# Kernel tuning notes

Hardware: AMD Instinct MI355X
Metric: run time of the kernel (lower is better)

The kernel has to match this reference:

```python
import jax, jax.numpy as jnp
import numpy as np

HID = 64        # HID_DIM of seq2seq encoder
NL = 2          # N_LAYERS
D = HID * NL    # dim_hidden = 128
TYPES = 16      # node op types; Input=0, Const=1
MAX_ET = 32     # max edge_type id
NUM_ROUNDS = 2


def _gru_cell(x, h, Wih, Whh, bih, bhh):
    # torch GRU gate ordering: r, z, n
    gi = x @ Wih.T + bih
    gh = h @ Whh.T + bhh
    ir, iz, inn = jnp.split(gi, 3, axis=-1)
    hr, hz, hn = jnp.split(gh, 3, axis=-1)
    r = jax.nn.sigmoid(ir + hr)
    z = jax.nn.sigmoid(iz + hz)
    n = jnp.tanh(inn + r * hn)
    return (1.0 - z) * n + z * h


def _posenc(n, d):
    pos = jnp.arange(n, dtype=jnp.float32)[:, None]
    i = jnp.arange(d // 2, dtype=jnp.float32)[None, :]
    inv = jnp.exp(-jnp.log(10000.0) * (2.0 * i / d))
    pe = jnp.zeros((n, d), jnp.float32)
    pe = pe.at[:, 0::2].set(jnp.sin(pos * inv))
    pe = pe.at[:, 1::2].set(jnp.cos(pos * inv))
    return pe


def _forward(x, edge_index, edge_type, sim_res, seq_len,
             enc_Wih0, enc_Whh0, enc_bih0, enc_bhh0,
             enc_Wih1, enc_Whh1, enc_bih1, enc_bhh1,
             Wq, Wk, Wv, op_emb, mlp_W1, mlp_b1, mlp_W2, mlp_b2,
             gru_Wih, gru_Whh, gru_bih, gru_bhh):
    N = x.shape[0]
    # --- seq2seq encode (2-layer GRU over time), computed for all nodes then masked ---
    xs = jnp.swapaxes(sim_res[:, :seq_len, :], 0, 1)  # [T, N, W]
    h0 = jnp.zeros((N, HID), sim_res.dtype)
    h1 = jnp.zeros((N, HID), sim_res.dtype)

    def step(carry, xt):
        h0, h1 = carry
        h0 = _gru_cell(xt, h0, enc_Wih0, enc_Whh0, enc_bih0, enc_bhh0)
        h1 = _gru_cell(h0, h1, enc_Wih1, enc_Whh1, enc_bih1, enc_bhh1)
        return (h0, h1), None

    (h0, h1), _ = jax.lax.scan(step, (h0, h1), xs)
    enc = jnp.concatenate([h0, h1], axis=-1)  # [N, D] = permute(1,0,2).flatten(1)
    mask = (x[:, 0] == 1) | (x[:, 1] == 1)    # Input | Const nodes
    node_emb = jnp.where(mask[:, None], enc, 0.0)

    src, dst = edge_index[0], edge_index[1]
    edge_op = jnp.argmax(x[dst], axis=1)       # [E]
    pe = _posenc(MAX_ET, D)
    edge_feat = pe[edge_type] + op_emb[edge_op]  # [E, D]
    scale = 1.0 / jnp.sqrt(jnp.float32(D))

    for _ in range(NUM_ROUNDS):
        kf = node_emb[src] + edge_feat         # [E, D]
        q = node_emb[dst] @ Wq.T
        k = kf @ Wk.T
        v = kf @ Wv.T
        score = jnp.sum(q * k, axis=-1) * scale  # [E]
        m = jax.ops.segment_max(score, dst, num_segments=N)
        ex = jnp.exp(score - m[dst])
        den = jax.ops.segment_sum(ex, dst, num_segments=N)
        alpha = ex / (den[dst] + 1e-9)
        aggr = jax.ops.segment_sum(alpha[:, None] * v, dst, num_segments=N)  # [N, D]
        aggr = jax.nn.relu(aggr @ mlp_W1.T + mlp_b1) @ mlp_W2.T + mlp_b2
        node_emb = _gru_cell(aggr, node_emb, gru_Wih, gru_Whh, gru_bih, gru_bhh)
    return node_emb


def setup_inputs() -> dict:
    key = jax.random.key(0)
    ks = jax.random.split(key, 24)
    N, E, T, W = 20000, 320000, 32, 32
    s = 0.05

    def g(k, shape):
        return jax.random.normal(k, shape, dtype=jnp.float32) * s

    node_type = jax.random.randint(ks[0], (N,), 0, TYPES)
    x = jax.nn.one_hot(node_type, TYPES, dtype=jnp.float32)
    edge_index = jax.random.randint(ks[1], (2, E), 0, N)
    edge_type = jax.random.randint(ks[2], (E,), 0, MAX_ET)
    sim_res = jax.random.uniform(ks[3], (N, T, W), dtype=jnp.float32)
    return {
        "x": x, "edge_index": edge_index, "edge_type": edge_type,
        "sim_res": sim_res, "seq_len": 32,
        "enc_Wih0": g(ks[4], (3 * HID, W)), "enc_Whh0": g(ks[5], (3 * HID, HID)),
        "enc_bih0": g(ks[6], (3 * HID,)), "enc_bhh0": g(ks[7], (3 * HID,)),
        "enc_Wih1": g(ks[8], (3 * HID, HID)), "enc_Whh1": g(ks[9], (3 * HID, HID)),
        "enc_bih1": g(ks[10], (3 * HID,)), "enc_bhh1": g(ks[11], (3 * HID,)),
        "Wq": g(ks[12], (D, D)), "Wk": g(ks[13], (D, D)), "Wv": g(ks[14], (D, D)),
        "op_emb": g(ks[15], (TYPES, D)),
        "mlp_W1": g(ks[16], (D, D)), "mlp_b1": g(ks[17], (D,)),
        "mlp_W2": g(ks[18], (D, D)), "mlp_b2": g(ks[19], (D,)),
        "gru_Wih": g(ks[20], (3 * D, D)), "gru_Whh": g(ks[21], (3 * D, D)),
        "gru_bih": g(ks[22], (3 * D,)), "gru_bhh": g(ks[23], (3 * D,)),
    }


def reference(x, edge_index, edge_type, sim_res, seq_len,
              enc_Wih0, enc_Whh0, enc_bih0, enc_bhh0,
              enc_Wih1, enc_Whh1, enc_bih1, enc_bhh1,
              Wq, Wk, Wv, op_emb, mlp_W1, mlp_b1, mlp_W2, mlp_b2,
              gru_Wih, gru_Whh, gru_bih, gru_bhh):
    return _forward(x, edge_index, edge_type, sim_res, seq_len,
                    enc_Wih0, enc_Whh0, enc_bih0, enc_bhh0,
                    enc_Wih1, enc_Whh1, enc_bih1, enc_bhh1,
                    Wq, Wk, Wv, op_emb, mlp_W1, mlp_b1, mlp_W2, mlp_b2,
                    gru_Wih, gru_Whh, gru_bih, gru_bhh)
```

## Files before the change

### kernel.cpp

```cpp
#include <hip/hip_runtime.h>

typedef unsigned int uint;
typedef unsigned short ushort;

typedef __attribute__((ext_vector_type(8))) short bf8;
typedef __attribute__((ext_vector_type(4))) float f32x4;
typedef _Float16 half_t;
typedef __attribute__((ext_vector_type(8))) half_t h8;

__device__ __forceinline__ ushort f2bf(float f){
  uint u = __builtin_bit_cast(uint, f);
  u = u + 0x7FFFu + ((u >> 16) & 1u);
  return (ushort)(u >> 16);
}
__device__ __forceinline__ float bfl(uint u){ return __builtin_bit_cast(float, u << 16); }
__device__ __forceinline__ float bfh(uint u){ return __builtin_bit_cast(float, u & 0xFFFF0000u); }
__device__ __forceinline__ uint pkhalf(float a, float b){
  ushort lo = __builtin_bit_cast(ushort, (half_t)a);
  ushort hi = __builtin_bit_cast(ushort, (half_t)b);
  return (uint)lo | ((uint)hi << 16);
}
__device__ __forceinline__ float sigmoidf_(float x){ return 1.0f/(1.0f + __expf(-x)); }
__device__ __forceinline__ float tanhf_(float x){
  x = fminf(15.0f, fmaxf(-15.0f, x));
  float t = __expf(-2.0f*x);
  return (1.0f - t)/(1.0f + t);
}
__device__ __forceinline__ f32x4 mfma_f16(h8 a, h8 b, f32x4 c){
  return __builtin_amdgcn_mfma_f32_16x16x32_f16(a, b, c, 0, 0, 0);
}
__device__ __forceinline__ f32x4 mfma_bf(bf8 a, bf8 b, f32x4 c){
  return __builtin_amdgcn_mfma_f32_16x16x32_bf16(a, b, c, 0, 0, 0);
}
__device__ __forceinline__ h8 ldw8(const float* p){
  f32x4 a = *(const f32x4*)p, b = *(const f32x4*)(p+4);
  h8 v;
  #pragma unroll
  for (int j=0;j<4;j++){ v[j] = (half_t)a[j]; v[4+j] = (half_t)b[j]; }
  return v;
}

__global__ __launch_bounds__(256) void k_prep(const float* __restrict__ x,
    const int* __restrict__ dst,
    int* __restrict__ typ, int* __restrict__ mlist, int* __restrict__ cnt,
    int* __restrict__ deg, float* __restrict__ Hf, ushort* __restrict__ Hb,
    int N, int E){
  int i = blockIdx.x*256 + threadIdx.x;
  int total = gridDim.x*256;
  if (i < N){
    const float* xr = x + (size_t)i*16;
    int t = 0;
    #pragma unroll
    for (int j=0;j<16;j++) if (xr[j] > 0.5f) t = j;
    typ[i] = t;
    if (t < 2){
      int p = atomicAdd(cnt, 1);
      mlist[p] = i;
    }
  }
  if (i < E) atomicAdd(&deg[dst[i]], 1);
  f32x4 z4 = (f32x4)0.0f;
  for (int j = i; j < N*32; j += total) ((f32x4*)Hf)[j] = z4;
  uint2 z2; z2.x = 0u; z2.y = 0u;
  for (int j = i; j < N*32; j += total) ((uint2*)Hb)[j] = z2;
}

__global__ __launch_bounds__(256) void k_cvt(
    const float* wq, const float* wk, const float* wv,
    const float* w1, const float* w2, const float* wih, const float* whh,
    const float* __restrict__ op_emb,
    ushort* oqkv, ushort* o1, ushort* o2, ushort* oih, ushort* ohh,
    ushort* __restrict__ EF){
  int i = blockIdx.x*256 + threadIdx.x;
  int stride = gridDim.x*256;
  for (int j=i; j<16384; j+=stride){
    oqkv[j]       = f2bf(wq[j]);
    oqkv[16384+j] = f2bf(wk[j]);
    oqkv[32768+j] = f2bf(wv[j]);
    o1[j] = f2bf(w1[j]);
    o2[j] = f2bf(w2[j]);
  }
  for (int j=i; j<49152; j+=stride){ oih[j]=f2bf(wih[j]); ohh[j]=f2bf(whh[j]); }
  for (int idx=i; idx<512*128; idx+=stride){
    int r = idx >> 7, d = idx & 127;
    int et = r >> 4, op = r & 15;
    int j = d >> 1;
    float inv = __expf(-0.1439115683f * (float)j);
    float ang = (float)et * inv;
    float v = (d & 1) ? __cosf(ang) : __sinf(ang);
    EF[idx] = f2bf(v + op_emb[op*128 + d]);
  }
}

template<int RELU, int HASBIAS>
__global__ __launch_bounds__(256) void k_gemm(
    const ushort* __restrict__ A, const ushort* __restrict__ B,
    const float* __restrict__ bias, ushort* __restrict__ C, int M, int N){
  int lane = threadIdx.x & 63, wv = threadIdx.x >> 6;
  int tM = blockIdx.x*64 + (wv>>1)*32;
  int tN = blockIdx.y*64 + (wv&1)*32;
  int r16 = lane & 15, kg = (lane>>4)*8;
  f32x4 acc[2][2];
  #pragma unroll
  for (int i=0;i<2;i++)
    #pragma unroll
    for (int j=0;j<2;j++) acc[i][j] = (f32x4)0.0f;
  #pragma unroll
  for (int k0=0;k0<128;k0+=32){
    bf8 a[2], b[2];
    #pragma unroll
    for (int i=0;i<2;i++){
      int row = tM + i*16 + r16; if (row > M-1) row = M-1;
      a[i] = *(const bf8*)(A + (size_t)row*128 + k0 + kg);
    }
    #pragma unroll
    for (int j=0;j<2;j++){
      int col = tN + j*16 + r16;
      b[j] = *(const bf8*)(B + (size_t)col*128 + k0 + kg);
    }
    #pragma unroll
    for (int i=0;i<2;i++)
      #pragma unroll
      for (int j=0;j<2;j++)
        acc[i][j] = __builtin_amdgcn_mfma_f32_16x16x32_bf16(a[i], b[j], acc[i][j], 0, 0, 0);
  }
  #pragma unroll
  for (int i=0;i<2;i++)
    #pragma unroll
    for (int j=0;j<2;j++){
      int col = tN + j*16 + r16;
      float bs = HASBIAS ? bias[col] : 0.0f;
      #pragma unroll
      for (int q=0;q<4;q++){
        int row = tM + i*16 + (lane>>4)*4 + q;
        if (row < M){
          float v = acc[i][j][q] + bs;
          if (RELU) v = fmaxf(v, 0.0f);
          C[(size_t)row*N + col] = f2bf(v);
        }
      }
    }
}

__global__ __launch_bounds__(512, 1) void k_enc4(
    const float* __restrict__ sim_res, const int* __restrict__ seqlen,
    const float* __restrict__ Wih0, const float* __restrict__ Whh0,
    const float* __restrict__ bih0, const float* __restrict__ bhh0,
    const float* __restrict__ Wih1, const float* __restrict__ Whh1,
    const float* __restrict__ bih1, const float* __restrict__ bhh1,
    const int* __restrict__ mlist, const int* __restrict__ cntp,
    float* __restrict__ Hf, ushort* __restrict__ Hb){
  int C = *cntp;
  int base = blockIdx.x * 16;
  if (C == 0 || base >= C) return;
  int tid = threadIdx.x;
  int w = tid >> 6, l = tid & 63;
  int node = l & 15, hi = l >> 4;
  int grp = w >> 2;
  int ws  = w & 3;

  __shared__ int nod[16];
  __shared__ __align__(16) float  Xs[16*32*32];
  __shared__ __align__(16) ushort H0h[2][16*64], H1h[2][16*64];

  if (tid < 16){
    int idx = base + tid;
    nod[tid] = mlist[idx < C ? idx : C-1];
  }
  for (int i = tid; i < 16*64; i += 512){
    H0h[0][i] = 0; H0h[1][i] = 0; H1h[0][i] = 0; H1h[1][i] = 0;
  }
  __syncthreads();

  for (int m = tid; m < 4096; m += 512){
    int nm = m >> 8, tt = (m >> 3) & 31, c = m & 7;
    int cs = c ^ (nm & 7);
    f32x4 v = *(const f32x4*)(sim_res + (size_t)nod[nm]*1024 + tt*32 + cs*4);
    *(f32x4*)(Xs + m*4) = v;
  }

  int rr = 16*ws + node;
  h8 zf;
  #pragma unroll
  for (int j=0;j<8;j++) zf[j] = (half_t)0.f;
  h8 Ai_r[2] = {zf, zf}, Ai_z[2] = {zf, zf}, Ai_n[2] = {zf, zf};
  h8 Ah_r[2], Ah_z[2], Ah_n[2];
  if (grp == 0){
    Ai_r[0] = ldw8(Wih0 + (size_t)rr*32        + hi*8);
    Ai_z[0] = ldw8(Wih0 + (size_t)(64+rr)*32   + hi*8);
    Ai_n[0] = ldw8(Wih0 + (size_t)(128+rr)*32  + hi*8);
    #pragma unroll
    for (int s=0;s<2;s++){
      Ah_r[s] = ldw8(Whh0 + (size_t)rr*64       + s*32 + hi*8);
      Ah_z[s] = ldw8(Whh0 + (size_t)(64+rr)*64  + s*32 + hi*8);
      Ah_n[s] = ldw8(Whh0 + (size_t)(128+rr)*64 + s*32 + hi*8);
    }
  } else {
    #pragma unroll
    for (int s=0;s<2;s++){
      Ai_r[s] = ldw8(Wih1 + (size_t)rr*64       + s*32 + hi*8);
      Ai_z[s] = ldw8(Wih1 + (size_t)(64+rr)*64  + s*32 + hi*8);
      Ai_n[s] = ldw8(Wih1 + (size_t)(128+rr)*64 + s*32 + hi*8);
      Ah_r[s] = ldw8(Whh1 + (size_t)rr*64       + s*32 + hi*8);
      Ah_z[s] = ldw8(Whh1 + (size_t)(64+rr)*64  + s*32 + hi*8);
      Ah_n[s] = ldw8(Whh1 + (size_t)(128+rr)*64 + s*32 + hi*8);
    }
  }
  const float* bi = grp ? bih1 : bih0;
  const float* bh = grp ? bhh1 : bhh0;
  float br[4], bz[4], bni[4], bnh[4];
  #pragma unroll
  for (int q=0;q<4;q++){
    int row = 16*ws + hi*4 + q;
    br[q]  = bi[row]      + bh[row];
    bz[q]  = bi[64+row]   + bh[64+row];
    bni[q] = bi[128+row];
    bnh[q] = bh[128+row];
  }

  int T = *seqlen; if (T > 32) T = 32; if (T < 0) T = 0;
  float hm[4] = {0.f, 0.f, 0.f, 0.f};

  const int swz = (node & 7) << 4;
  const int wo  = node * 128;
  const int wba = 32*ws + 8*hi;
  const int rd0 = wo + ((16*hi) ^ swz);
  const int rd1 = wo + ((64 + 16*hi) ^ swz);
  const int xc0 = (2*hi)   ^ (node & 7);
  const int xc1 = (2*hi+1) ^ (node & 7);
  const float* xrow = Xs + node*1024;

  __syncthreads();

  for (int k = 0; k <= T; ++k){
    int cur = k & 1;
    bool act = grp ? (k >= 1) : (k < T);
    if (act){
      h8 in0 = zf, in1 = zf, st0, st1;
      if (grp == 0){
        f32x4 xa = *(const f32x4*)(xrow + k*32 + xc0*4);
        f32x4 xb = *(const f32x4*)(xrow + k*32 + xc1*4);
        #pragma unroll
        for (int j=0;j<4;j++){ in0[j] = (half_t)xa[j]; in0[4+j] = (half_t)xb[j]; }
        st0 = *(const h8*)((const char*)H0h[cur] + rd0);
        st1 = *(const h8*)((const char*)H0h[cur] + rd1);
      } else {
        in0 = *(const h8*)((const char*)H0h[cur] + rd0);
        in1 = *(const h8*)((const char*)H0h[cur] + rd1);
        st0 = *(const h8*)((const char*)H1h[cur] + rd0);
        st1 = *(const h8*)((const char*)H1h[cur] + rd1);
      }
      f32x4 ar = {br[0],br[1],br[2],br[3]};
      f32x4 az = {bz[0],bz[1],bz[2],bz[3]};
      f32x4 an = {bni[0],bni[1],bni[2],bni[3]};
      f32x4 hn = {bnh[0],bnh[1],bnh[2],bnh[3]};
      ar = mfma_f16(Ai_r[0], in0, ar);
      az = mfma_f16(Ai_z[0], in0, az);
      an = mfma_f16(Ai_n[0], in0, an);
      if (grp){
        ar = mfma_f16(Ai_r[1], in1, ar);
        az = mfma_f16(Ai_z[1], in1, az);
        an = mfma_f16(Ai_n[1], in1, an);
      }
      ar = mfma_f16(Ah_r[0], st0, ar); ar = mfma_f16(Ah_r[1], st1, ar);
      az = mfma_f16(Ah_z[0], st0, az); az = mfma_f16(Ah_z[1], st1, az);
      hn = mfma_f16(Ah_n[0], st0, hn); hn = mfma_f16(Ah_n[1], st1, hn);
      #pragma unroll
      for (int q=0;q<4;q++){
        float r = sigmoidf_(ar[q]);
        float z = sigmoidf_(az[q]);
        float n = tanhf_(an[q] + r*hn[q]);
        hm[q] = (1.f - z)*n + z*hm[q];
      }
      char* outb = grp ? (char*)H1h[cur^1] : (char*)H0h[cur^1];
      *(uint*)(outb + wo + ( wba      ^ swz)) = pkhalf(hm[0], hm[1]);
      *(uint*)(outb + wo + ((wba + 4) ^ swz)) = pkhalf(hm[2], hm[3]);
    }
    __syncthreads();
  }

  if (base + node < C){
    int nd = nod[node];
    int off = grp ? 64 : 0;
    #pragma unroll
    for (int q=0;q<4;q++){
      int j = off + 16*ws + hi*4 + q;
      Hf[(size_t)nd*128 + j] = hm[q];
      Hb[(size_t)nd*128 + j] = f2bf(hm[q]);
    }
  }
}

__global__ __launch_bounds__(1024) void k_scan(const int* __restrict__ deg,
    int* __restrict__ rowptr, int* __restrict__ cursor, int N){
  __shared__ int wsum[16];
  __shared__ int carry_s;
  int tid = threadIdx.x, lane = tid & 63, wid = tid >> 6;
  if (tid == 0) carry_s = 0;
  __syncthreads();
  int nch = (N + 1023) / 1024;
  for (int c=0; c<nch; ++c){
    int i = c*1024 + tid;
    int v = (i < N) ? deg[i] : 0;
    int x = v;
    #pragma unroll
    for (int off=1; off<64; off<<=1){
      int t = __shfl_up(x, off, 64);
      if (lane >= off) x += t;
    }
    if (lane == 63) wsum[wid] = x;
    __syncthreads();
    int base = carry_s;
    int woff = 0;
    for (int w2=0; w2<wid; ++w2) woff += wsum[w2];
    int excl = base + woff + x - v;
    if (i < N){ rowptr[i] = excl; cursor[i] = excl; }
    __syncthreads();
    if (tid == 0){
      int s = 0;
      for (int w2=0; w2<16; ++w2) s += wsum[w2];
      carry_s = base + s;
    }
    __syncthreads();
  }
  if (tid == 0) rowptr[N] = carry_s;
}

__global__ __launch_bounds__(256) void k_scatter(const int* __restrict__ src,
    const int* __restrict__ dst, const int* __restrict__ etype, const int* __restrict__ typ,
    int* __restrict__ cursor, int* __restrict__ es_src, int* __restrict__ es_tab, int E){
  int e = blockIdx.x*256 + threadIdx.x;
  if (e < E){
    int d = dst[e];
    int pos = atomicAdd(&cursor[d], 1);
    es_src[pos] = src[e];
    es_tab[pos] = etype[e]*16 + typ[d];
  }
}

__global__ __launch_bounds__(256) void k_attn(
    const uint* __restrict__ QKV, const uint* __restrict__ KVT,
    const int* __restrict__ rowptr, const int* __restrict__ es_src, const int* __restrict__ es_tab,
    uint* __restrict__ aggr, int N){
  int w = threadIdx.x >> 6, lane = threadIdx.x & 63;
  int dst = blockIdx.x*4 + w;
  if (dst >= N) return;
  uint qu = QKV[(size_t)dst*192 + lane];
  const float scale = 0.08838834764831845f;
  float q0 = bfl(qu)*scale, q1 = bfh(qu)*scale;
  int s0 = rowptr[dst], s1 = rowptr[dst+1];
  float m = -1e30f, den = 0.f, a0 = 0.f, a1 = 0.f;
  int p = s0;
  for (; p + 2 <= s1; p += 2){
    int srcA = es_src[p],   tbA = es_tab[p];
    int srcB = es_src[p+1], tbB = es_tab[p+1];
    uint kuA = QKV[(size_t)srcA*192 + 64 + lane],  ktA = KVT[(size_t)tbA*128 + lane];
    uint vuA = QKV[(size_t)srcA*192 + 128 + lane], vtA = KVT[(size_t)tbA*128 + 64 + lane];
    uint kuB = QKV[(size_t)srcB*192 + 64 + lane],  ktB = KVT[(size_t)tbB*128 + lane];
    uint vuB = QKV[(size_t)srcB*192 + 128 + lane], vtB = KVT[(size_t)tbB*128 + 64 + lane];
    float sA = q0*(bfl(kuA)+bfl(ktA)) + q1*(bfh(kuA)+bfh(ktA));
    float sB = q0*(bfl(kuB)+bfl(ktB)) + q1*(bfh(kuB)+bfh(ktB));
    #pragma unroll
    for (int off=32; off; off>>=1){
      sA += __shfl_xor(sA, off);
      sB += __shfl_xor(sB, off);
    }
    float nm = fmaxf(m, fmaxf(sA, sB));
    float c  = __expf(m - nm);
    float pA = __expf(sA - nm), pB = __expf(sB - nm);
    den = den*c + pA + pB;
    a0  = a0*c + pA*(bfl(vuA)+bfl(vtA)) + pB*(bfl(vuB)+bfl(vtB));
    a1  = a1*c + pA*(bfh(vuA)+bfh(vtA)) + pB*(bfh(vuB)+bfh(vtB));
    m = nm;
  }
  for (; p < s1; ++p){
    int src = es_src[p], tb = es_tab[p];
    uint ku = QKV[(size_t)src*192 + 64 + lane],  kt = KVT[(size_t)tb*128 + lane];
    uint vu = QKV[(size_t)src*192 + 128 + lane], vt = KVT[(size_t)tb*128 + 64 + lane];
    float s = q0*(bfl(ku)+bfl(kt)) + q1*(bfh(ku)+bfh(kt));
    #pragma unroll
    for (int off=32; off; off>>=1) s += __shfl_xor(s, off);
    float nm = fmaxf(m, s);
    float c  = __expf(m - nm);
    float pw = __expf(s - nm);
    den = den*c + pw;
    a0  = a0*c + pw*(bfl(vu)+bfl(vt));
    a1  = a1*c + pw*(bfh(vu)+bfh(vt));
    m = nm;
  }
  float inv = 1.0f/(den + 1e-9f);
  a0 *= inv; a1 *= inv;
  aggr[(size_t)dst*64 + lane] = ((uint)f2bf(a1) << 16) | (uint)f2bf(a0);
}

__global__ __launch_bounds__(256) void k_fused(
    const ushort* __restrict__ Ag,
    const ushort* __restrict__ W1b, const float* __restrict__ b1,
    const ushort* __restrict__ W2b, const float* __restrict__ b2,
    const ushort* __restrict__ Wih, const ushort* __restrict__ Whh,
    const float* __restrict__ bih, const float* __restrict__ bhh,
    const ushort* Hbf, const float* Hf_in,
    float* Hf_out, ushort* Hb_out, int M){
  int lane = threadIdx.x & 63, wv = threadIdx.x >> 6;
  int nb = blockIdx.x * 32;
  int r16 = lane & 15, kq = lane >> 4;

  __shared__ __align__(16) ushort T[32*128];

  {
    f32x4 acc[2][2];
    #pragma unroll
    for (int i=0;i<2;i++)
      #pragma unroll
      for (int j=0;j<2;j++) acc[i][j] = (f32x4)0.0f;
    #pragma unroll
    for (int ks=0; ks<4; ++ks){
      bf8 a[2], b[2];
      #pragma unroll
      for (int i=0;i<2;i++){
        int row = nb + i*16 + r16; if (row > M-1) row = M-1;
        a[i] = *(const bf8*)(Ag + (size_t)row*128 + ks*32 + kq*8);
      }
      #pragma unroll
      for (int j=0;j<2;j++)
        b[j] = *(const bf8*)(W1b + (size_t)(wv*32 + j*16 + r16)*128 + ks*32 + kq*8);
      #pragma unroll
      for (int i=0;i<2;i++)
        #pragma unroll
        for (int j=0;j<2;j++) acc[i][j] = mfma_bf(a[i], b[j], acc[i][j]);
    }
    #pragma unroll
    for (int i=0;i<2;i++)
      #pragma unroll
      for (int j=0;j<2;j++){
        int col = wv*32 + j*16 + r16;
        float bs = b1[col];
        #pragma unroll
        for (int q=0;q<4;q++){
          int row = i*16 + kq*4 + q;
          float v = fmaxf(acc[i][j][q] + bs, 0.0f);
          *(ushort*)((char*)T + ((row*256 + col*2) ^ ((row&7)<<4))) = f2bf(v);
        }
      }
  }
  __syncthreads();

  {
    f32x4 acc[2][2];
    #pragma unroll
    for (int i=0;i<2;i++)
      #pragma unroll
      for (int j=0;j<2;j++) acc[i][j] = (f32x4)0.0f;
    #pragma unroll
    for (int ks=0; ks<4; ++ks){
      bf8 a[2], b[2];
      #pragma unroll
      for (int i=0;i<2;i++){
        int row = i*16 + r16;
        a[i] = *(const bf8*)((const char*)T + row*256 + ((ks*64 + kq*16) ^ ((row&7)<<4)));
      }
      #pragma unroll
      for (int j=0;j<2;j++)
        b[j] = *(const bf8*)(W2b + (size_t)(wv*32 + j*16 + r16)*128 + ks*32 + kq*8);
      #pragma unroll
      for (int i=0;i<2;i++)
        #pragma unroll
        for (int j=0;j<2;j++) acc[i][j] = mfma_bf(a[i], b[j], acc[i][j]);
    }
    __syncthreads();
    #pragma unroll
    for (int i=0;i<2;i++)
      #pragma unroll
      for (int j=0;j<2;j++){
        int col = wv*32 + j*16 + r16;
        float bs = b2[col];
        #pragma unroll
        for (int q=0;q<4;q++){
          int row = i*16 + kq*4 + q;
          *(ushort*)((char*)T + ((row*256 + col*2) ^ ((row&7)<<4))) = f2bf(acc[i][j][q] + bs);
        }
      }
  }
  __syncthreads();

  f32x4 ar[2][2], az[2][2], ani[2][2], anh[2][2];
  #pragma unroll
  for (int i=0;i<2;i++)
    #pragma unroll
    for (int p2=0;p2<2;p2++){
      ar[i][p2] = (f32x4)0.0f; az[i][p2] = (f32x4)0.0f;
      ani[i][p2] = (f32x4)0.0f; anh[i][p2] = (f32x4)0.0f;
    }
  #pragma unroll
  for (int ks=0; ks<4; ++ks){
    bf8 ax[2], ah[2];
    #pragma unroll
    for (int i=0;i<2;i++){
      int row = i*16 + r16;
      ax[i] = *(const bf8*)((const char*)T + row*256 + ((ks*64 + kq*16) ^ ((row&7)<<4)));
      int grow = nb + row; if (grow > M-1) grow = M-1;
      ah[i] = *(const bf8*)(Hbf + (size_t)grow*128 + ks*32 + kq*8);
    }
    #pragma unroll
    for (int p2=0;p2<2;p2++){
      int cb = wv*32 + p2*16 + r16;
      bf8 wri = *(const bf8*)(Wih + (size_t)cb*128        + ks*32 + kq*8);
      bf8 wrh = *(const bf8*)(Whh + (size_t)cb*128        + ks*32 + kq*8);
      bf8 wzi = *(const bf8*)(Wih + (size_t)(128+cb)*128  + ks*32 + kq*8);
      bf8 wzh = *(const bf8*)(Whh + (size_t)(128+cb)*128  + ks*32 + kq*8);
      bf8 wni = *(const bf8*)(Wih + (size_t)(256+cb)*128  + ks*32 + kq*8);
      bf8 wnh = *(const bf8*)(Whh + (size_t)(256+cb)*128  + ks*32 + kq*8);
      #pragma unroll
      for (int i=0;i<2;i++){
        ar[i][p2]  = mfma_bf(ax[i], wri, ar[i][p2]);
        ar[i][p2]  = mfma_bf(ah[i], wrh, ar[i][p2]);
        az[i][p2]  = mfma_bf(ax[i], wzi, az[i][p2]);
        az[i][p2]  = mfma_bf(ah[i], wzh, az[i][p2]);
        ani[i][p2] = mfma_bf(ax[i], wni, ani[i][p2]);
        anh[i][p2] = mfma_bf(ah[i], wnh, anh[i][p2]);
      }
    }
  }
  __syncthreads();
  #pragma unroll
  for (int i=0;i<2;i++)
    #pragma unroll
    for (int p2=0;p2<2;p2++){
      int jcol = wv*32 + p2*16 + r16;
      float br_  = bih[jcol]     + bhh[jcol];
      float bz_  = bih[128+jcol] + bhh[128+jcol];
      float bni_ = bih[256+jcol];
      float bnh_ = bhh[256+jcol];
      #pragma unroll
      for (int q=0;q<4;q++){
        int node = nb + i*16 + kq*4 + q;
        if (node < M){
          float r = sigmoidf_(ar[i][p2][q] + br_);
          float z = sigmoidf_(az[i][p2][q] + bz_);
          float n = tanhf_(ani[i][p2][q] + bni_ + r*(anh[i][p2][q] + bnh_));
          float h = Hf_in[(size_t)node*128 + jcol];
          float o = (1.f - z)*n + z*h;
          Hf_out[(size_t)node*128 + jcol] = o;
          Hb_out[(size_t)node*128 + jcol] = f2bf(o);
        }
      }
    }
}

extern "C" void kernel_launch(void* const* d_in, const int* in_sizes, int n_in,
                              void* d_out, int out_size, void* d_ws, size_t ws_size,
                              hipStream_t stream){
  const float* x       = (const float*)d_in[0];
  const int*   ei      = (const int*)d_in[1];
  const int*   etype   = (const int*)d_in[2];
  const float* sim_res = (const float*)d_in[3];
  const int*   seqlen  = (const int*)d_in[4];
  const float* eWih0 = (const float*)d_in[5];
  const float* eWhh0 = (const float*)d_in[6];
  const float* ebih0 = (const float*)d_in[7];
  const float* ebhh0 = (const float*)d_in[8];
  const float* eWih1 = (const float*)d_in[9];
  const float* eWhh1 = (const float*)d_in[10];
  const float* ebih1 = (const float*)d_in[11];
  const float* ebhh1 = (const float*)d_in[12];
  const float* Wq = (const float*)d_in[13];
  const float* Wk = (const float*)d_in[14];
  const float* Wv = (const float*)d_in[15];
  const float* op_emb = (const float*)d_in[16];
  const float* W1 = (const float*)d_in[17];
  const float* b1 = (const float*)d_in[18];
  const float* W2 = (const float*)d_in[19];
  const float* b2 = (const float*)d_in[20];
  const float* gWih = (const float*)d_in[21];
  const float* gWhh = (const float*)d_in[22];
  const float* gbih = (const float*)d_in[23];
  const float* gbhh = (const float*)d_in[24];

  const int N = in_sizes[0] / 16;
  const int E = in_sizes[2];

  char* p = (char*)d_ws;
  auto take = [&](size_t b)->void*{ void* r = (void*)p; p += (b + 255) & ~(size_t)255; return r; };

  float*  Hf    = (float*) take((size_t)N*128*4);
  ushort* Hb    = (ushort*)take((size_t)N*128*2);
  ushort* QKV   = (ushort*)take((size_t)N*384*2);
  ushort* Ag    = (ushort*)take((size_t)N*128*2);
  ushort* EF    = (ushort*)take((size_t)512*128*2);
  ushort* KVtab = (ushort*)take((size_t)512*256*2);
  ushort* wqkv  = (ushort*)take((size_t)3*16384*2);
  ushort* w1_b  = (ushort*)take((size_t)16384*2);
  ushort* w2_b  = (ushort*)take((size_t)16384*2);
  ushort* wih_b = (ushort*)take((size_t)49152*2);
  ushort* whh_b = (ushort*)take((size_t)49152*2);
  int* typ    = (int*)take((size_t)N*4);
  int* mlist  = (int*)take((size_t)N*4);
  int* cnt    = (int*)take(256);
  int* deg    = (int*)take((size_t)N*4);
  int* rowptr = (int*)take((size_t)(N+1)*4);
  int* cursor = (int*)take((size_t)N*4);
  int* es_src = (int*)take((size_t)E*4);
  int* es_tab = (int*)take((size_t)E*4);

  hipMemsetAsync(cnt, 0, 4, stream);
  hipMemsetAsync(deg, 0, (size_t)N*4, stream);

  int gE = (E + 255) / 256;
  k_prep<<<gE, 256, 0, stream>>>(x, ei + E, typ, mlist, cnt, deg, Hf, Hb, N, E);
  k_cvt<<<256, 256, 0, stream>>>(Wq, Wk, Wv, W1, W2, gWih, gWhh, op_emb,
                                 wqkv, w1_b, w2_b, wih_b, whh_b, EF);
  k_gemm<0,0><<<dim3(8,4), 256, 0, stream>>>(EF, wqkv + 16384, nullptr, KVtab, 512, 256);
  k_enc4<<<(N+15)/16, 512, 0, stream>>>(sim_res, seqlen, eWih0, eWhh0, ebih0, ebhh0,
                                        eWih1, eWhh1, ebih1, ebhh1, mlist, cnt, Hf, Hb);
  k_scan<<<1, 1024, 0, stream>>>(deg, rowptr, cursor, N);
  k_scatter<<<gE, 256, 0, stream>>>(ei, ei + E, etype, typ, cursor, es_src, es_tab, E);

  dim3 gq((N+63)/64, 6);
  for (int r=0; r<2; ++r){
    k_gemm<0,0><<<gq, 256, 0, stream>>>(Hb, wqkv, nullptr, QKV, N, 384);
    k_attn<<<(N+3)/4, 256, 0, stream>>>((const uint*)QKV, (const uint*)KVtab,
                                        rowptr, es_src, es_tab, (uint*)Ag, N);
    float* hf_out = (r == 1) ? (float*)d_out : Hf;
    k_fused<<<(N+31)/32, 256, 0, stream>>>(Ag, w1_b, b1, w2_b, b2,
                                           wih_b, whh_b, gbih, gbhh,
                                           Hb, Hf, hf_out, Hb, N);
  }
}
```

Baseline: 314.7 us.

## Unroll attention edge loop by four and split fused MLP-GRU across eight waves

The attention kernel now handles four edges per iteration instead of two. This puts more independent gathers and shuffle reductions in flight per wave. The fused MLP+GRU kernel goes from 4 to 8 waves per block (512 threads), with each wave owning 16 output columns instead of 32. It also prefetches the aggregated rows, the hidden-state rows and the previous fp32 hidden values into registers at kernel start. This aims to raise parallelism and hide global-load latency, at the cost of higher register pressure (launch bounds 512,2) and duplicated activation loads across waves.

New measurement: 309.0 us. About the same (-1.8%).

```diff
diff --git a/kernel.cpp b/kernel.cpp
--- a/kernel.cpp
+++ b/kernel.cpp
@@ -351,26 +351,39 @@
   int s0 = rowptr[dst], s1 = rowptr[dst+1];
   float m = -1e30f, den = 0.f, a0 = 0.f, a1 = 0.f;
   int p = s0;
-  for (; p + 2 <= s1; p += 2){
-    int srcA = es_src[p],   tbA = es_tab[p];
-    int srcB = es_src[p+1], tbB = es_tab[p+1];
-    uint kuA = QKV[(size_t)srcA*192 + 64 + lane],  ktA = KVT[(size_t)tbA*128 + lane];
-    uint vuA = QKV[(size_t)srcA*192 + 128 + lane], vtA = KVT[(size_t)tbA*128 + 64 + lane];
-    uint kuB = QKV[(size_t)srcB*192 + 64 + lane],  ktB = KVT[(size_t)tbB*128 + lane];
-    uint vuB = QKV[(size_t)srcB*192 + 128 + lane], vtB = KVT[(size_t)tbB*128 + 64 + lane];
-    float sA = q0*(bfl(kuA)+bfl(ktA)) + q1*(bfh(kuA)+bfh(ktA));
-    float sB = q0*(bfl(kuB)+bfl(ktB)) + q1*(bfh(kuB)+bfh(ktB));
+  for (; p + 4 <= s1; p += 4){
+    int se[4], te[4];
+    #pragma unroll
+    for (int e=0;e<4;e++){ se[e] = es_src[p+e]; te[e] = es_tab[p+e]; }
+    uint ku[4], kt[4], vu[4], vt[4];
+    #pragma unroll
+    for (int e=0;e<4;e++){
+      ku[e] = QKV[(size_t)se[e]*192 + 64 + lane];
+      kt[e] = KVT[(size_t)te[e]*128 + lane];
+      vu[e] = QKV[(size_t)se[e]*192 + 128 + lane];
+      vt[e] = KVT[(size_t)te[e]*128 + 64 + lane];
+    }
+    float s[4];
+    #pragma unroll
+    for (int e=0;e<4;e++)
+      s[e] = q0*(bfl(ku[e])+bfl(kt[e])) + q1*(bfh(ku[e])+bfh(kt[e]));
     #pragma unroll
     for (int off=32; off; off>>=1){
-      sA += __shfl_xor(sA, off);
-      sB += __shfl_xor(sB, off);
-    }
-    float nm = fmaxf(m, fmaxf(sA, sB));
+      #pragma unroll
+      for (int e=0;e<4;e++) s[e] += __shfl_xor(s[e], off);
+    }
+    float nm = fmaxf(fmaxf(m, fmaxf(s[0], s[1])), fmaxf(s[2], s[3]));
     float c  = __expf(m - nm);
-    float pA = __expf(sA - nm), pB = __expf(sB - nm);
-    den = den*c + pA + pB;
-    a0  = a0*c + pA*(bfl(vuA)+bfl(vtA)) + pB*(bfl(vuB)+bfl(vtB));
-    a1  = a1*c + pA*(bfh(vuA)+bfh(vtA)) + pB*(bfh(vuB)+bfh(vtB));
+    float pw[4];
+    #pragma unroll
+    for (int e=0;e<4;e++) pw[e] = __expf(s[e] - nm);
+    den = den*c + pw[0] + pw[1] + pw[2] + pw[3];
+    a0 = a0*c; a1 = a1*c;
+    #pragma unroll
+    for (int e=0;e<4;e++){
+      a0 += pw[e]*(bfl(vu[e])+bfl(vt[e]));
+      a1 += pw[e]*(bfh(vu[e])+bfh(vt[e]));
+    }
     m = nm;
   }
   for (; p < s1; ++p){
@@ -393,7 +406,7 @@
   aggr[(size_t)dst*64 + lane] = ((uint)f2bf(a1) << 16) | (uint)f2bf(a0);
 }
 
-__global__ __launch_bounds__(256) void k_fused(
+__global__ __launch_bounds__(512, 2) void k_fused(
     const ushort* __restrict__ Ag,
     const ushort* __restrict__ W1b, const float* __restrict__ b1,
     const ushort* __restrict__ W2b, const float* __restrict__ b2,
@@ -401,148 +414,132 @@
     const float* __restrict__ bih, const float* __restrict__ bhh,
     const ushort* Hbf, const float* Hf_in,
     float* Hf_out, ushort* Hb_out, int M){
-  int lane = threadIdx.x & 63, wv = threadIdx.x >> 6;
+  int lane = threadIdx.x & 63, w = threadIdx.x >> 6;
   int nb = blockIdx.x * 32;
   int r16 = lane & 15, kq = lane >> 4;
+  const int col = w*16 + r16;
 
   __shared__ __align__(16) ushort T[32*128];
 
+  bf8 agld[2][4], ahld[2][4];
+  #pragma unroll
+  for (int i=0;i<2;i++){
+    int grow = nb + i*16 + r16; if (grow > M-1) grow = M-1;
+    #pragma unroll
+    for (int ks=0;ks<4;ks++){
+      agld[i][ks] = *(const bf8*)(Ag  + (size_t)grow*128 + ks*32 + kq*8);
+      ahld[i][ks] = *(const bf8*)(Hbf + (size_t)grow*128 + ks*32 + kq*8);
+    }
+  }
+  float hprev[2][4];
+  #pragma unroll
+  for (int i=0;i<2;i++)
+    #pragma unroll
+    for (int q=0;q<4;q++){
+      int node = nb + i*16 + kq*4 + q;
+      hprev[i][q] = Hf_in[(size_t)(node < M ? node : M-1)*128 + col];
+    }
+
   {
-    f32x4 acc[2][2];
-    #pragma unroll
-    for (int i=0;i<2;i++)
-      #pragma unroll
-      for (int j=0;j<2;j++) acc[i][j] = (f32x4)0.0f;
+    f32x4 a0 = (f32x4)0.0f, a1v = (f32x4)0.0f;
     #pragma unroll
     for (int ks=0; ks<4; ++ks){
-      bf8 a[2], b[2];
-      #pragma unroll
-      for (int i=0;i<2;i++){
-        int row = nb + i*16 + r16; if (row > M-1) row = M-1;
-        a[i] = *(const bf8*)(Ag + (size_t)row*128 + ks*32 + kq*8);
+      bf8 wb = *(const bf8*)(W1b + (size_t)col*128 + ks*32 + kq*8);
+      a0  = mfma_bf(agld[0][ks], wb, a0);
+      a1v = mfma_bf(agld[1][ks], wb, a1v);
+    }
+    float bs = b1[col];
+    #pragma unroll
+    for (int q=0;q<4;q++){
+      int row0 = kq*4 + q, row1 = 16 + kq*4 + q;
+      *(ushort*)((char*)T + ((row0*256 + col*2) ^ ((row0&7)<<4))) = f2bf(fmaxf(a0[q]  + bs, 0.0f));
+      *(ushort*)((char*)T + ((row1*256 + col*2) ^ ((row1&7)<<4))) = f2bf(fmaxf(a1v[q] + bs, 0.0f));
+    }
+  }
+  __syncthreads();
+
+  {
+    f32x4 a0 = (f32x4)0.0f, a1v = (f32x4)0.0f;
+    #pragma unroll
+    for (int ks=0; ks<4; ++ks){
+      bf8 wb = *(const bf8*)(W2b + (size_t)col*128 + ks*32 + kq*8);
+      bf8 ax0, ax1;
+      {
+        int row = r16;
+        ax0 = *(const bf8*)((const char*)T + row*256 + ((ks*64 + kq*16) ^ ((row&7)<<4)));
       }
-      #pragma unroll
-      for (int j=0;j<2;j++)
-        b[j] = *(const bf8*)(W1b + (size_t)(wv*32 + j*16 + r16)*128 + ks*32 + kq*8);
-      #pragma unroll
-      for (int i=0;i<2;i++)
-        #pragma unroll
-        for (int j=0;j<2;j++) acc[i][j] = mfma_bf(a[i], b[j], acc[i][j]);
-    }
-    #pragma unroll
-    for (int i=0;i<2;i++)
-      #pragma unroll
-      for (int j=0;j<2;j++){
-        int col = wv*32 + j*16 + r16;
-        float bs = b1[col];
-        #pragma unroll
-        for (int q=0;q<4;q++){
-          int row = i*16 + kq*4 + q;
-          float v = fmaxf(acc[i][j][q] + bs, 0.0f);
-          *(ushort*)((char*)T + ((row*256 + col*2) ^ ((row&7)<<4))) = f2bf(v);
-        }
+      {
+        int row = 16 + r16;
+        ax1 = *(const bf8*)((const char*)T + row*256 + ((ks*64 + kq*16) ^ ((row&7)<<4)));
       }
+      a0  = mfma_bf(ax0, wb, a0);
+      a1v = mfma_bf(ax1, wb, a1v);
+    }
+    __syncthreads();
+    float bs = b2[col];
+    #pragma unroll
+    for (int q=0;q<4;q++){
+      int row0 = kq*4 + q, row1 = 16 + kq*4 + q;
+      *(ushort*)((char*)T + ((row0*256 + col*2) ^ ((row0&7)<<4))) = f2bf(a0[q]  + bs);
+      *(ushort*)((char*)T + ((row1*256 + col*2) ^ ((row1&7)<<4))) = f2bf(a1v[q] + bs);
+    }
   }
   __syncthreads();
 
-  {
-    f32x4 acc[2][2];
-    #pragma unroll
-    for (int i=0;i<2;i++)
-      #pragma unroll
-      for (int j=0;j<2;j++) acc[i][j] = (f32x4)0.0f;
-    #pragma unroll
-    for (int ks=0; ks<4; ++ks){
-      bf8 a[2], b[2];
-      #pragma unroll
-      for (int i=0;i<2;i++){
-        int row = i*16 + r16;
-        a[i] = *(const bf8*)((const char*)T + row*256 + ((ks*64 + kq*16) ^ ((row&7)<<4)));
-      }
-      #pragma unroll
-      for (int j=0;j<2;j++)
-        b[j] = *(const bf8*)(W2b + (size_t)(wv*32 + j*16 + r16)*128 + ks*32 + kq*8);
-      #pragma unroll
-      for (int i=0;i<2;i++)
-        #pragma unroll
-        for (int j=0;j<2;j++) acc[i][j] = mfma_bf(a[i], b[j], acc[i][j]);
-    }
-    __syncthreads();
-    #pragma unroll
-    for (int i=0;i<2;i++)
-      #pragma unroll
-      for (int j=0;j<2;j++){
-        int col = wv*32 + j*16 + r16;
-        float bs = b2[col];
-        #pragma unroll
-        for (int q=0;q<4;q++){
-          int row = i*16 + kq*4 + q;
-          *(ushort*)((char*)T + ((row*256 + col*2) ^ ((row&7)<<4))) = f2bf(acc[i][j][q] + bs);
-        }
-      }
-  }
-  __syncthreads();
-
-  f32x4 ar[2][2], az[2][2], ani[2][2], anh[2][2];
+  f32x4 ar[2], az[2], ani[2], anh[2];
+  #pragma unroll
+  for (int i=0;i<2;i++){
+    ar[i] = (f32x4)0.0f; az[i] = (f32x4)0.0f;
+    ani[i] = (f32x4)0.0f; anh[i] = (f32x4)0.0f;
+  }
+  #pragma unroll
+  for (int ks=0; ks<4; ++ks){
+    int off = ks*32 + kq*8;
+    bf8 wri = *(const bf8*)(Wih + (size_t)col*128       + off);
+    bf8 wrh = *(const bf8*)(Whh + (size_t)col*128       + off);
+    bf8 wzi = *(const bf8*)(Wih + (size_t)(128+col)*128 + off);
+    bf8 wzh = *(const bf8*)(Whh + (size_t)(128+col)*128 + off);
+    bf8 wni = *(const bf8*)(Wih + (size_t)(256+col)*128 + off);
+    bf8 wnh = *(const bf8*)(Whh + (size_t)(256+col)*128 + off);
+    bf8 ax0, ax1;
+    {
+      int row = r16;
+      ax0 = *(const bf8*)((const char*)T + row*256 + ((ks*64 + kq*16) ^ ((row&7)<<4)));
+    }
+    {
+      int row = 16 + r16;
+      ax1 = *(const bf8*)((const char*)T + row*256 + ((ks*64 + kq*16) ^ ((row&7)<<4)));
+    }
+    ar[0]  = mfma_bf(ax0,         wri, ar[0]);
+    ar[0]  = mfma_bf(ahld[0][ks], wrh, ar[0]);
+    az[0]  = mfma_bf(ax0,         wzi, az[0]);
+    az[0]  = mfma_bf(ahld[0][ks], wzh, az[0]);
+    ani[0] = mfma_bf(ax0,         wni, ani[0]);
+    anh[0] = mfma_bf(ahld[0][ks], wnh, anh[0]);
+    ar[1]  = mfma_bf(ax1,         wri, ar[1]);
+    ar[1]  = mfma_bf(ahld[1][ks], wrh, ar[1]);
+    az[1]  = mfma_bf(ax1,         wzi, az[1]);
+    az[1]  = mfma_bf(ahld[1][ks], wzh, az[1]);
+    ani[1] = mfma_bf(ax1,         wni, ani[1]);
+    anh[1] = mfma_bf(ahld[1][ks], wnh, anh[1]);
+  }
+  float br_  = bih[col]     + bhh[col];
+  float bz_  = bih[128+col] + bhh[128+col];
+  float bni_ = bih[256+col];
+  float bnh_ = bhh[256+col];
   #pragma unroll
   for (int i=0;i<2;i++)
     #pragma unroll
-    for (int p2=0;p2<2;p2++){
-      ar[i][p2] = (f32x4)0.0f; az[i][p2] = (f32x4)0.0f;
-      ani[i][p2] = (f32x4)0.0f; anh[i][p2] = (f32x4)0.0f;
-    }
-  #pragma unroll
-  for (int ks=0; ks<4; ++ks){
-    bf8 ax[2], ah[2];
-    #pragma unroll
-    for (int i=0;i<2;i++){
-      int row = i*16 + r16;
-      ax[i] = *(const bf8*)((const char*)T + row*256 + ((ks*64 + kq*16) ^ ((row&7)<<4)));
-      int grow = nb + row; if (grow > M-1) grow = M-1;
-      ah[i] = *(const bf8*)(Hbf + (size_t)grow*128 + ks*32 + kq*8);
-    }
-    #pragma unroll
-    for (int p2=0;p2<2;p2++){
-      int cb = wv*32 + p2*16 + r16;
-      bf8 wri = *(const bf8*)(Wih + (size_t)cb*128        + ks*32 + kq*8);
-      bf8 wrh = *(const bf8*)(Whh + (size_t)cb*128        + ks*32 + kq*8);
-      bf8 wzi = *(const bf8*)(Wih + (size_t)(128+cb)*128  + ks*32 + kq*8);
-      bf8 wzh = *(const bf8*)(Whh + (size_t)(128+cb)*128  + ks*32 + kq*8);
-      bf8 wni = *(const bf8*)(Wih + (size_t)(256+cb)*128  + ks*32 + kq*8);
-      bf8 wnh = *(const bf8*)(Whh + (size_t)(256+cb)*128  + ks*32 + kq*8);
-      #pragma unroll
-      for (int i=0;i<2;i++){
-        ar[i][p2]  = mfma_bf(ax[i], wri, ar[i][p2]);
-        ar[i][p2]  = mfma_bf(ah[i], wrh, ar[i][p2]);
-        az[i][p2]  = mfma_bf(ax[i], wzi, az[i][p2]);
-        az[i][p2]  = mfma_bf(ah[i], wzh, az[i][p2]);
-        ani[i][p2] = mfma_bf(ax[i], wni, ani[i][p2]);
-        anh[i][p2] = mfma_bf(ah[i], wnh, anh[i][p2]);
-      }
-    }
-  }
-  __syncthreads();
-  #pragma unroll
-  for (int i=0;i<2;i++)
-    #pragma unroll
-    for (int p2=0;p2<2;p2++){
-      int jcol = wv*32 + p2*16 + r16;
-      float br_  = bih[jcol]     + bhh[jcol];
-      float bz_  = bih[128+jcol] + bhh[128+jcol];
-      float bni_ = bih[256+jcol];
-      float bnh_ = bhh[256+jcol];
-      #pragma unroll
-      for (int q=0;q<4;q++){
-        int node = nb + i*16 + kq*4 + q;
-        if (node < M){
-          float r = sigmoidf_(ar[i][p2][q] + br_);
-          float z = sigmoidf_(az[i][p2][q] + bz_);
-          float n = tanhf_(ani[i][p2][q] + bni_ + r*(anh[i][p2][q] + bnh_));
-          float h = Hf_in[(size_t)node*128 + jcol];
-          float o = (1.f - z)*n + z*h;
-          Hf_out[(size_t)node*128 + jcol] = o;
-          Hb_out[(size_t)node*128 + jcol] = f2bf(o);
-        }
+    for (int q=0;q<4;q++){
+      int node = nb + i*16 + kq*4 + q;
+      if (node < M){
+        float r = sigmoidf_(ar[i][q] + br_);
+        float z = sigmoidf_(az[i][q] + bz_);
+        float n = tanhf_(ani[i][q] + bni_ + r*(anh[i][q] + bnh_));
+        float h = hprev[i][q];
+        float o = (1.f - z)*n + z*h;
+        Hf_out[(size_t)node*128 + col] = o;
+        Hb_out[(size_t)node*128 + col] = f2bf(o);
       }
     }
 }
@@ -621,7 +618,7 @@
     k_attn<<<(N+3)/4, 256, 0, stream>>>((const uint*)QKV, (const uint*)KVtab,
                                         rowptr, es_src, es_tab, (uint*)Ag, N);
     float* hf_out = (r == 1) ? (float*)d_out : Hf;
-    k_fused<<<(N+31)/32, 256, 0, stream>>>(Ag, w1_b, b1, w2_b, b2,
+    k_fused<<<(N+31)/32, 512, 0, stream>>>(Ag, w1_b, b1, w2_b, b2,
                                            wih_b, whh_b, gbih, gbhh,
                                            Hb, Hf, hf_out, Hb, N);
   }
```
